# Performance work log

Hardware: AMD Instinct MI355X
Metric: run time of the kernel (lower is better)

## Reference

```python
import jax, jax.numpy as jnp
import numpy as np


def setup_inputs() -> dict:
    key = jax.random.key(0)
    ks = jax.random.split(key, 6)
    b, c, h, w = 8, 256, 48, 48
    return {
        "qry_fts": jax.random.normal(ks[0], (b, c, h, w), dtype=jnp.float32),
        "mask_fts": jax.random.normal(ks[1], (b, c, h, w), dtype=jnp.float32),
        "fts": jax.random.normal(ks[2], (b, c, h, w), dtype=jnp.float32),
        "Wq": jax.random.normal(ks[3], (c, c), dtype=jnp.float32) * (1.0 / np.sqrt(c)),
        "Wk": jax.random.normal(ks[4], (c, c), dtype=jnp.float32) * (1.0 / np.sqrt(c)),
        "Wv": jax.random.normal(ks[5], (c, c), dtype=jnp.float32) * (1.0 / np.sqrt(c)),
        "mu": jnp.full((1,), 0.5, dtype=jnp.float32),
    }


def reference(qry_fts, mask_fts, fts, Wq, Wk, Wv, mu):
    b, c, h, w = qry_fts.shape
    # flatten spatial dims to tokens: [b, N, c], N = h*w
    q_tok = qry_fts.reshape(b, c, h * w).transpose(0, 2, 1)
    m_tok = mask_fts.reshape(b, c, h * w).transpose(0, 2, 1)
    f_tok = fts.reshape(b, c, h * w).transpose(0, 2, 1)

    # torch Linear(no bias): y = x @ W^T with W [out,in]
    Q = jnp.einsum("bnc,dc->bnd", q_tok, Wq)
    K1 = jnp.einsum("bnc,dc->bnd", f_tok, Wk)
    K2 = jnp.einsum("bnc,dc->bnd", m_tok, Wk)
    V = jnp.einsum("bnc,dc->bnd", f_tok, Wv)

    A1 = jax.nn.softmax(jnp.einsum("bqd,bkd->bqk", Q, K1), axis=-1)
    A2 = jax.nn.softmax(jnp.einsum("bqd,bkd->bqk", Q, K2), axis=-1)
    A = (A1 * 0.5 + A2 * mu[0]) / (0.5 + mu[0])

    att = jnp.einsum("bqk,bkd->bqd", A, V)  # [b, N, c]
    att = att.reshape(b, h, w, c).transpose(0, 3, 1, 2)
    return qry_fts + att
```

## Files before the change

kernel.cpp:

```cpp
#include <hip/hip_runtime.h>
#include <math.h>

#define BB 8
#define CC 256
#define NTOK 2304
#define NP 72
#define LOG2E 1.4426950408889634f
#define BIAS2 72.134752f

typedef __attribute__((ext_vector_type(4))) float f32x4;
typedef __attribute__((ext_vector_type(8))) short s16x8;
typedef __attribute__((ext_vector_type(4))) short s16x4;

__device__ inline unsigned short f2bf(float x) {
  unsigned u = __builtin_bit_cast(unsigned, x);
  return (unsigned short)((u + 0x7FFFu + ((u >> 16) & 1u)) >> 16);
}
__device__ inline unsigned short f2h(float x) {
  _Float16 h = (_Float16)x;
  return __builtin_bit_cast(unsigned short, h);
}

__device__ inline void async16(void* lds, const void* g) {
  __builtin_amdgcn_global_load_lds(
      (const __attribute__((address_space(1))) unsigned int*)g,
      (__attribute__((address_space(3))) unsigned int*)lds, 16, 0, 0);
}

__global__ __launch_bounds__(256)
void prep_kernel(const float* __restrict__ X, unsigned short* __restrict__ Xt) {
  __shared__ float Ls[64][65];
  const int t = threadIdx.x;
  const int n0 = blockIdx.x * 64, c0 = blockIdx.y * 64, b = blockIdx.z;
  const float* Xb = X + (size_t)b * CC * NTOK;
  unsigned short* Yb = Xt + (size_t)b * CC * NTOK;

  #pragma unroll
  for (int rr = 0; rr < 16; rr++) {
    int cl = rr * 4 + (t >> 6);
    Ls[cl][t & 63] = Xb[(size_t)(c0 + cl) * NTOK + n0 + (t & 63)];
  }
  __syncthreads();
  #pragma unroll
  for (int rr = 0; rr < 8; rr++) {
    int nl = rr * 8 + (t >> 5);
    int cl = (t & 31) * 2;
    unsigned v = (unsigned)f2h(Ls[cl][nl]) | ((unsigned)f2h(Ls[cl + 1][nl]) << 16);
    *(unsigned*)((char*)Yb + ((size_t)(n0 + nl) * CC + c0 + cl) * 2) = v;
  }
}

__global__ __launch_bounds__(256)
void wconv_kernel(const float* __restrict__ Wq, const float* __restrict__ Wk,
                  const float* __restrict__ Wv, unsigned short* __restrict__ Wqh,
                  unsigned short* __restrict__ Wkh, unsigned short* __restrict__ Wvh) {
  const float* src = (blockIdx.y == 0) ? Wq : (blockIdx.y == 1) ? Wk : Wv;
  unsigned short* dst = (blockIdx.y == 0) ? Wqh : (blockIdx.y == 1) ? Wkh : Wvh;
  int gi = (blockIdx.x * 256 + threadIdx.x) * 4;
  f32x4 v = *(const f32x4*)(src + gi);
  s16x4 o;
  #pragma unroll
  for (int i = 0; i < 4; i++) o[i] = (short)f2h(v[i]);
  *(s16x4*)(dst + gi) = o;
}

template<int MODE>
__global__ __launch_bounds__(256, 2)
void gemm_kernel(const unsigned short* __restrict__ Xt, const unsigned short* __restrict__ Wh,
                 unsigned short* __restrict__ Y) {
  __shared__ alignas(16) char smem[32768];

  const int t = threadIdx.x;
  const int w = t >> 6, l = t & 63, g = l >> 4, c = l & 15;
  const int bid = blockIdx.x;
  const int b = bid & 7, nt = bid >> 3;
  const int n0w = nt * 64 + w * 16;
  const size_t bo = (size_t)b * CC * NTOK;

  const char* Xb = (const char*)(Xt + bo);
  const char* Wb = (const char*)Wh;
  char* Yb = (char*)(Y + (MODE == 2 ? bo : bo));

  int koff[4], cdst[4];
  #pragma unroll
  for (int j = 0; j < 4; j++) {
    int ck = w + 4 * j;
    int row = ck * 2 + (l >> 5);
    koff[j] = row * 512 + (((l & 31) * 16) ^ ((row & 7) << 4));
    cdst[j] = ck * 1024 + l * 16;
  }
  int kxor[8];
  #pragma unroll
  for (int dc = 0; dc < 8; dc++)
    kxor[dc] = (dc * 64 + g * 16) ^ ((c & 7) << 4);

  s16x8 xa[8];
  #pragma unroll
  for (int dc = 0; dc < 8; dc++)
    xa[dc] = *(const s16x8*)(Xb + (n0w + c) * 512 + dc * 64 + g * 16);

  f32x4 acc[16];

#define STAGE_W(WB, TILE)                                            \
  do {                                                               \
    _Pragma("unroll")                                                \
    for (int j_ = 0; j_ < 4; j_++)                                   \
      async16((WB) + cdst[j_], Wb + (TILE) * 16384 + koff[j_]);      \
  } while (0)

  STAGE_W(smem, 0);
  __syncthreads();

  #pragma unroll
  for (int ph = 0; ph < 8; ph++) {
    char* cur = smem + (ph & 1) * 16384;
    if (ph < 7) STAGE_W(smem + ((ph & 1) ^ 1) * 16384, ph + 1);
    __builtin_amdgcn_s_setprio(1);
    #pragma unroll
    for (int s = 0; s < 2; s++) {
      const char* Kt = cur + (s * 16 + c) * 512;
      f32x4 sa = (f32x4){0.f, 0.f, 0.f, 0.f};
      #pragma unroll
      for (int dc = 0; dc < 8; dc++) {
        s16x8 wf = *(const s16x8*)(Kt + kxor[dc]);
        sa = __builtin_amdgcn_mfma_f32_16x16x32_f16(xa[dc], wf, sa, 0, 0, 0);
      }
      acc[ph * 2 + s] = sa;
    }
    __builtin_amdgcn_s_setprio(0);
    __syncthreads();
  }
#undef STAGE_W

  if (MODE == 0 || MODE == 1) {
    unsigned short* Ws = (unsigned short*)(smem + w * 8192);
    #pragma unroll
    for (int dt = 0; dt < 16; dt++)
      #pragma unroll
      for (int j = 0; j < 4; j++) {
        float v = (MODE == 0) ? acc[dt][j] * LOG2E : acc[dt][j];
        Ws[(g * 4 + j) * 256 + dt * 16 + c] = f2h(v);
      }
    #pragma unroll
    for (int r = 0; r < 16; r++) {
      s16x4 v = *(const s16x4*)&Ws[r * 256 + l * 4];
      *(s16x4*)(Yb + (size_t)(n0w + r) * 512 + l * 8) = v;
    }
  } else {
    unsigned short* Vs = (unsigned short*)(smem + w * 8192);
    #pragma unroll
    for (int dt = 0; dt < 16; dt++) {
      s16x4 pv;
      #pragma unroll
      for (int j = 0; j < 4; j++) pv[j] = (short)f2bf(acc[dt][j]);
      *(s16x4*)&Vs[c * 20 + g * 4] = pv;
      s16x4 vv = *(const s16x4*)&Vs[(l >> 2) * 20 + (l & 3) * 4];
      *(s16x4*)(Yb + (size_t)(dt * 16 + (l >> 2)) * 4608 + (size_t)(n0w + (l & 3) * 4) * 2) = vv;
    }
  }
}

__global__ __launch_bounds__(256, 2)
void attn_kernel(const unsigned short* __restrict__ Qf, const unsigned short* __restrict__ K1,
                 const unsigned short* __restrict__ K2, const unsigned short* __restrict__ Vt,
                 const float* __restrict__ qry, const float* __restrict__ mup,
                 float* __restrict__ out) {
  __shared__ alignas(16) char smem[79360];
  char* const kb0 = smem;
  char* const kb1 = smem + 16384;

  const int t = threadIdx.x;
  const int w = t >> 6, l = t & 63, g = l >> 4, c = l & 15;
  const int bid = blockIdx.x;
  const int b = bid & 7, qt = bid >> 3;
  const int q0 = qt * 64 + w * 16;
  const size_t bo = (size_t)b * CC * NTOK;

  const char* Qb  = (const char*)(Qf + bo);
  const char* K1b = (const char*)(K1 + bo);
  const char* K2b = (const char*)(K2 + bo);
  const char* Vtb = (const char*)(Vt + bo);

  float* const Pe0 = (float*)(smem + 65536 + w * 3456);
  float* const Pe1 = Pe0 + 288;
  float* const Pod = Pe0 + 576;

  int koff[2], voff[2], cdst[2];
  #pragma unroll
  for (int j = 0; j < 2; j++) {
    int ck = w + 4 * j;
    int tok = ck * 2 + (l >> 5);
    koff[j] = tok * 512 + (((l & 31) * 16) ^ ((tok & 7) << 4));
    voff[j] = (ck * 32 + (l >> 1)) * 4608 + (l & 1) * 16;
    cdst[j] = ck * 1024 + l * 16;
  }

  int kxor[8];
  #pragma unroll
  for (int dc = 0; dc < 8; dc++)
    kxor[dc] = (dc * 64 + g * 16) ^ ((c & 7) << 4);

  s16x8 qf[8];
  #pragma unroll
  for (int dc = 0; dc < 8; dc++)
    qf[dc] = *(const s16x8*)(Qb + (q0 + c) * 512 + dc * 64 + g * 16);

  f32x4 a1[16], a2[16];
  #pragma unroll
  for (int dt = 0; dt < 16; dt++) {
    a1[dt] = (f32x4){0.f, 0.f, 0.f, 0.f};
    a2[dt] = (f32x4){0.f, 0.f, 0.f, 0.f};
  }
  float lr1[4] = {0.f, 0.f, 0.f, 0.f};
  float lr2[4] = {0.f, 0.f, 0.f, 0.f};

#define STAGE_K(KB, TILE)                                                  \
  do {                                                                     \
    _Pragma("unroll")                                                      \
    for (int pp_ = 0; pp_ < 2; pp_++) {                                    \
      const char* ks_ = (pp_ ? K2b : K1b) + (size_t)(TILE) * 8192;         \
      async16((KB) + pp_ * 8192 + cdst[0], ks_ + koff[0]);                 \
      async16((KB) + pp_ * 8192 + cdst[1], ks_ + koff[1]);                 \
    }                                                                      \
  } while (0)

#define STAGE_V(VB, PAIR)                                                  \
  do {                                                                     \
    _Pragma("unroll")                                                      \
    for (int h_ = 0; h_ < 2; h_++) {                                       \
      const char* vs_ = Vtb + (PAIR) * 64 + h_ * 32;                       \
      async16((VB) + h_ * 8192 + cdst[0], vs_ + voff[0]);                  \
      async16((VB) + h_ * 8192 + cdst[1], vs_ + voff[1]);                  \
    }                                                                      \
  } while (0)

  STAGE_K(kb0, 0);
  STAGE_V(smem + 32768, 0);
  __syncthreads();

  for (int p = 0; p < NP; p++) {
    char* vcur = smem + 32768 + (p & 1) * 16384;
    char* vnxt = smem + 32768 + ((p & 1) ^ 1) * 16384;

    STAGE_K(kb1, 2 * p + 1);
    #pragma unroll
    for (int pp = 0; pp < 2; pp++) {
      const char* Kt = kb0 + pp * 8192 + c * 512;
      f32x4 s = (f32x4){0.f, 0.f, 0.f, 0.f};
      __builtin_amdgcn_s_setprio(1);
      #pragma unroll
      for (int dc = 0; dc < 8; dc++) {
        s16x8 kf = *(const s16x8*)(Kt + kxor[dc]);
        s = __builtin_amdgcn_mfma_f32_16x16x32_f16(qf[dc], kf, s, 0, 0, 0);
      }
      __builtin_amdgcn_s_setprio(0);
      float* lr = pp ? lr2 : lr1;
      float* Pe = pp ? Pe1 : Pe0;
      #pragma unroll
      for (int j = 0; j < 4; j++) {
        float pv = exp2f(s[j] - BIAS2);
        lr[j] += pv;
        Pe[(g * 4 + j) * 18 + c] = pv;
      }
    }
    __syncthreads();

    if (p + 1 < NP) {
      STAGE_K(kb0, 2 * p + 2);
      STAGE_V(vnxt, p + 1);
    }
    s16x8 pa0, pa1;
    #pragma unroll
    for (int pp = 0; pp < 2; pp++) {
      const char* Kt = kb1 + pp * 8192 + c * 512;
      f32x4 s = (f32x4){0.f, 0.f, 0.f, 0.f};
      __builtin_amdgcn_s_setprio(1);
      #pragma unroll
      for (int dc = 0; dc < 8; dc++) {
        s16x8 kf = *(const s16x8*)(Kt + kxor[dc]);
        s = __builtin_amdgcn_mfma_f32_16x16x32_f16(qf[dc], kf, s, 0, 0, 0);
      }
      __builtin_amdgcn_s_setprio(0);
      float* lr = pp ? lr2 : lr1;
      #pragma unroll
      for (int j = 0; j < 4; j++) {
        float pv = exp2f(s[j] - BIAS2);
        lr[j] += pv;
        Pod[(g * 4 + j) * 18 + c] = pv;
      }
      const float* src = ((g < 2) ? (pp ? Pe1 : Pe0) : Pod) + c * 18 + (g & 1) * 8;
      s16x8 v;
      #pragma unroll
      for (int i = 0; i < 8; i++) v[i] = (short)f2bf(src[i]);
      if (pp == 0) pa0 = v; else pa1 = v;
    }
    {
      const char* vbase = vcur + ((g >= 2) ? 8192 : 0) + c * 32 + (g & 1) * 16;
      __builtin_amdgcn_s_setprio(1);
      #pragma unroll
      for (int dt = 0; dt < 16; dt++) {
        s16x8 vf = *(const s16x8*)(vbase + dt * 512);
        a1[dt] = __builtin_amdgcn_mfma_f32_16x16x32_bf16(pa0, vf, a1[dt], 0, 0, 0);
        a2[dt] = __builtin_amdgcn_mfma_f32_16x16x32_bf16(pa1, vf, a2[dt], 0, 0, 0);
      }
      __builtin_amdgcn_s_setprio(0);
    }
    __syncthreads();
  }
#undef STAGE_K
#undef STAGE_V

  #pragma unroll
  for (int j = 0; j < 4; j++) {
    #pragma unroll
    for (int off = 1; off < 16; off <<= 1) {
      lr1[j] += __shfl_xor(lr1[j], off);
      lr2[j] += __shfl_xor(lr2[j], off);
    }
  }
  const float mu = mup[0];
  const float cw1 = 0.5f / (0.5f + mu);
  const float cw2 = mu / (0.5f + mu);
  float r1[4], r2[4];
  #pragma unroll
  for (int j = 0; j < 4; j++) { r1[j] = cw1 / lr1[j]; r2[j] = cw2 / lr2[j]; }

  float* Ws = (float*)(smem + w * 4352);
  const int q = l & 15, ds = l >> 4;
  #pragma unroll
  for (int ch = 0; ch < 4; ch++) {
    #pragma unroll
    for (int dtp = 0; dtp < 4; dtp++) {
      const int dt = ch * 4 + dtp;
      #pragma unroll
      for (int j = 0; j < 4; j++)
        Ws[(g * 4 + j) * 68 + dtp * 16 + c] = a1[dt][j] * r1[j] + a2[dt][j] * r2[j];
    }
    #pragma unroll
    for (int i = 0; i < 16; i++) {
      int d = ch * 64 + i * 4 + ds;
      size_t gi = bo + (size_t)d * NTOK + q0 + q;
      out[gi] = qry[gi] + Ws[q * 68 + i * 4 + ds];
    }
  }
}

extern "C" void kernel_launch(void* const* d_in, const int* in_sizes, int n_in,
                              void* d_out, int out_size, void* d_ws, size_t ws_size,
                              hipStream_t stream) {
  const float* qry  = (const float*)d_in[0];
  const float* mask = (const float*)d_in[1];
  const float* fts  = (const float*)d_in[2];
  const float* Wq   = (const float*)d_in[3];
  const float* Wk   = (const float*)d_in[4];
  const float* Wv   = (const float*)d_in[5];
  const float* mu   = (const float*)d_in[6];
  float* out = (float*)d_out;

  const size_t SZ = (size_t)BB * CC * NTOK;
  unsigned short* Xtq = (unsigned short*)d_ws;
  unsigned short* Xtm = Xtq + SZ;
  unsigned short* Xtf = Xtq + 2 * SZ;
  unsigned short* Qw  = Xtq + 3 * SZ;
  unsigned short* K1w = Xtq + 4 * SZ;
  unsigned short* K2w = Xtq + 5 * SZ;
  unsigned short* Vtw = Xtq + 6 * SZ;
  unsigned short* Wqh = Xtq + 7 * SZ;
  unsigned short* Wkh = Wqh + CC * CC;
  unsigned short* Wvh = Wkh + CC * CC;

  dim3 pg(NTOK / 64, CC / 64, BB);
  prep_kernel<<<pg, 256, 0, stream>>>(qry,  Xtq);
  prep_kernel<<<pg, 256, 0, stream>>>(mask, Xtm);
  prep_kernel<<<pg, 256, 0, stream>>>(fts,  Xtf);
  wconv_kernel<<<dim3(64, 3), 256, 0, stream>>>(Wq, Wk, Wv, Wqh, Wkh, Wvh);

  const int GG = BB * (NTOK / 64);
  gemm_kernel<0><<<GG, 256, 0, stream>>>(Xtq, Wqh, Qw);
  gemm_kernel<1><<<GG, 256, 0, stream>>>(Xtf, Wkh, K1w);
  gemm_kernel<1><<<GG, 256, 0, stream>>>(Xtm, Wkh, K2w);
  gemm_kernel<2><<<GG, 256, 0, stream>>>(Xtf, Wvh, Vtw);

  attn_kernel<<<GG, 256, 0, stream>>>(Qw, K1w, K2w, Vtw, qry, mu, out);
}
```

Baseline: 256.9 us.

## Split attention over key halves and add a combine kernel

The attention kernel now splits the key range into two halves, which doubles the grid from 288 to 576 blocks and gives better occupancy across the CUs. Each block writes unnormalized partial outputs in bf16 plus row sums to workspace, and a new combine kernel sums the halves, normalizes, mixes the two softmaxes and adds the residual. This works because softmax uses a fixed bias instead of a running max. The V LDS layout also gets an XOR swizzle to cut bank conflicts. The cost is extra global traffic for the partials, one more launch, and a second bf16 rounding of the partial outputs.

```diff
diff --git a/kernel.cpp b/kernel.cpp
--- a/kernel.cpp
+++ b/kernel.cpp
@@ -4,7 +4,7 @@
 #define BB 8
 #define CC 256
 #define NTOK 2304
-#define NP 72
+#define NPL 36
 #define LOG2E 1.4426950408889634f
 #define BIAS2 72.134752f
 
@@ -15,6 +15,9 @@
 __device__ inline unsigned short f2bf(float x) {
   unsigned u = __builtin_bit_cast(unsigned, x);
   return (unsigned short)((u + 0x7FFFu + ((u >> 16) & 1u)) >> 16);
+}
+__device__ inline float bf2f(unsigned short h) {
+  return __builtin_bit_cast(float, (unsigned)h << 16);
 }
 __device__ inline unsigned short f2h(float x) {
   _Float16 h = (_Float16)x;
@@ -79,7 +82,7 @@
 
   const char* Xb = (const char*)(Xt + bo);
   const char* Wb = (const char*)Wh;
-  char* Yb = (char*)(Y + (MODE == 2 ? bo : bo));
+  char* Yb = (char*)(Y + bo);
 
   int koff[4], cdst[4];
   #pragma unroll
@@ -163,8 +166,8 @@
 __global__ __launch_bounds__(256, 2)
 void attn_kernel(const unsigned short* __restrict__ Qf, const unsigned short* __restrict__ K1,
                  const unsigned short* __restrict__ K2, const unsigned short* __restrict__ Vt,
-                 const float* __restrict__ qry, const float* __restrict__ mup,
-                 float* __restrict__ out) {
+                 unsigned short* __restrict__ pa1, unsigned short* __restrict__ pa2,
+                 float* __restrict__ lb) {
   __shared__ alignas(16) char smem[79360];
   char* const kb0 = smem;
   char* const kb1 = smem + 16384;
@@ -172,7 +175,9 @@
   const int t = threadIdx.x;
   const int w = t >> 6, l = t & 63, g = l >> 4, c = l & 15;
   const int bid = blockIdx.x;
-  const int b = bid & 7, qt = bid >> 3;
+  const int b = bid & 7;
+  const int r0 = bid >> 3;
+  const int qt = r0 % 36, half = r0 / 36;
   const int q0 = qt * 64 + w * 16;
   const size_t bo = (size_t)b * CC * NTOK;
 
@@ -191,7 +196,7 @@
     int ck = w + 4 * j;
     int tok = ck * 2 + (l >> 5);
     koff[j] = tok * 512 + (((l & 31) * 16) ^ ((tok & 7) << 4));
-    voff[j] = (ck * 32 + (l >> 1)) * 4608 + (l & 1) * 16;
+    voff[j] = (ck * 32 + (l >> 1)) * 4608 + (((l & 1) ^ ((l >> 3) & 1)) << 4);
     cdst[j] = ck * 1024 + l * 16;
   }
 
@@ -234,15 +239,18 @@
     }                                                                      \
   } while (0)
 
-  STAGE_K(kb0, 0);
-  STAGE_V(smem + 32768, 0);
+  const int tb = half * 72;
+  const int pb = half * 36;
+
+  STAGE_K(kb0, tb);
+  STAGE_V(smem + 32768, pb);
   __syncthreads();
 
-  for (int p = 0; p < NP; p++) {
+  for (int p = 0; p < NPL; p++) {
     char* vcur = smem + 32768 + (p & 1) * 16384;
     char* vnxt = smem + 32768 + ((p & 1) ^ 1) * 16384;
 
-    STAGE_K(kb1, 2 * p + 1);
+    STAGE_K(kb1, tb + 2 * p + 1);
     #pragma unroll
     for (int pp = 0; pp < 2; pp++) {
       const char* Kt = kb0 + pp * 8192 + c * 512;
@@ -265,11 +273,11 @@
     }
     __syncthreads();
 
-    if (p + 1 < NP) {
-      STAGE_K(kb0, 2 * p + 2);
-      STAGE_V(vnxt, p + 1);
-    }
-    s16x8 pa0, pa1;
+    if (p + 1 < NPL) {
+      STAGE_K(kb0, tb + 2 * p + 2);
+      STAGE_V(vnxt, pb + p + 1);
+    }
+    s16x8 pa0, pa1r;
     #pragma unroll
     for (int pp = 0; pp < 2; pp++) {
       const char* Kt = kb1 + pp * 8192 + c * 512;
@@ -292,16 +300,17 @@
       s16x8 v;
       #pragma unroll
       for (int i = 0; i < 8; i++) v[i] = (short)f2bf(src[i]);
-      if (pp == 0) pa0 = v; else pa1 = v;
+      if (pp == 0) pa0 = v; else pa1r = v;
     }
     {
-      const char* vbase = vcur + ((g >= 2) ? 8192 : 0) + c * 32 + (g & 1) * 16;
+      const char* vbase = vcur + ((g >= 2) ? 8192 : 0) + c * 32 +
+                          ((((g & 1) ^ ((c >> 2) & 1))) << 4);
       __builtin_amdgcn_s_setprio(1);
       #pragma unroll
       for (int dt = 0; dt < 16; dt++) {
         s16x8 vf = *(const s16x8*)(vbase + dt * 512);
         a1[dt] = __builtin_amdgcn_mfma_f32_16x16x32_bf16(pa0, vf, a1[dt], 0, 0, 0);
-        a2[dt] = __builtin_amdgcn_mfma_f32_16x16x32_bf16(pa1, vf, a2[dt], 0, 0, 0);
+        a2[dt] = __builtin_amdgcn_mfma_f32_16x16x32_bf16(pa1r, vf, a2[dt], 0, 0, 0);
       }
       __builtin_amdgcn_s_setprio(0);
     }
@@ -318,30 +327,75 @@
       lr2[j] += __shfl_xor(lr2[j], off);
     }
   }
-  const float mu = mup[0];
-  const float cw1 = 0.5f / (0.5f + mu);
-  const float cw2 = mu / (0.5f + mu);
-  float r1[4], r2[4];
-  #pragma unroll
-  for (int j = 0; j < 4; j++) { r1[j] = cw1 / lr1[j]; r2[j] = cw2 / lr2[j]; }
-
+  const int pqidx = (half * 8 + b) * 36 + qt;
+  if (c == 0) {
+    #pragma unroll
+    for (int j = 0; j < 4; j++) {
+      int row = w * 16 + g * 4 + j;
+      lb[pqidx * 64 + row] = lr1[j];
+      lb[36864 + pqidx * 64 + row] = lr2[j];
+    }
+  }
+
+  unsigned short* const pb1 = pa1 + (size_t)pqidx * 16384;
+  unsigned short* const pb2 = pa2 + (size_t)pqidx * 16384;
   float* Ws = (float*)(smem + w * 4352);
   const int q = l & 15, ds = l >> 4;
   #pragma unroll
   for (int ch = 0; ch < 4; ch++) {
     #pragma unroll
-    for (int dtp = 0; dtp < 4; dtp++) {
-      const int dt = ch * 4 + dtp;
-      #pragma unroll
-      for (int j = 0; j < 4; j++)
-        Ws[(g * 4 + j) * 68 + dtp * 16 + c] = a1[dt][j] * r1[j] + a2[dt][j] * r2[j];
-    }
-    #pragma unroll
-    for (int i = 0; i < 16; i++) {
-      int d = ch * 64 + i * 4 + ds;
-      size_t gi = bo + (size_t)d * NTOK + q0 + q;
-      out[gi] = qry[gi] + Ws[q * 68 + i * 4 + ds];
-    }
+    for (int pth = 0; pth < 2; pth++) {
+      const f32x4* ap = pth ? a2 : a1;
+      unsigned short* pdst = pth ? pb2 : pb1;
+      #pragma unroll
+      for (int dtp = 0; dtp < 4; dtp++) {
+        const int dt = ch * 4 + dtp;
+        #pragma unroll
+        for (int j = 0; j < 4; j++)
+          Ws[(g * 4 + j) * 68 + dtp * 16 + c] = ap[dt][j];
+      }
+      #pragma unroll
+      for (int i = 0; i < 16; i++) {
+        int d = ch * 64 + i * 4 + ds;
+        pdst[d * 64 + w * 16 + q] = f2bf(Ws[q * 68 + i * 4 + ds]);
+      }
+      __builtin_amdgcn_s_barrier();
+    }
+  }
+}
+
+__global__ __launch_bounds__(256)
+void combine_kernel(const unsigned short* __restrict__ pa1, const unsigned short* __restrict__ pa2,
+                    const float* __restrict__ lb, const float* __restrict__ qry,
+                    const float* __restrict__ mup, float* __restrict__ out) {
+  const int bid = blockIdx.x;
+  const int b = bid & 7, qt = bid >> 3;
+  const int t = threadIdx.x;
+  const int q = t & 63, dr = t >> 6;
+  const size_t bo = (size_t)b * CC * NTOK;
+  const int q0 = qt * 64;
+
+  const int i0 = (0 * 8 + b) * 36 + qt;
+  const int i1 = (1 * 8 + b) * 36 + qt;
+  float l1 = lb[i0 * 64 + q] + lb[i1 * 64 + q];
+  float l2 = lb[36864 + i0 * 64 + q] + lb[36864 + i1 * 64 + q];
+  const float mu = mup[0];
+  const float w1 = 0.5f / (0.5f + mu) / l1;
+  const float w2 = mu / (0.5f + mu) / l2;
+
+  const unsigned short* p10 = pa1 + (size_t)i0 * 16384;
+  const unsigned short* p11 = pa1 + (size_t)i1 * 16384;
+  const unsigned short* p20 = pa2 + (size_t)i0 * 16384;
+  const unsigned short* p21 = pa2 + (size_t)i1 * 16384;
+
+  #pragma unroll
+  for (int i = 0; i < 64; i++) {
+    int d = dr * 64 + i;
+    int off = d * 64 + q;
+    float av1 = bf2f(p10[off]) + bf2f(p11[off]);
+    float av2 = bf2f(p20[off]) + bf2f(p21[off]);
+    size_t gi = bo + (size_t)d * NTOK + q0 + q;
+    out[gi] = qry[gi] + av1 * w1 + av2 * w2;
   }
 }
 
@@ -358,14 +412,18 @@
   float* out = (float*)d_out;
 
   const size_t SZ = (size_t)BB * CC * NTOK;
-  unsigned short* Xtq = (unsigned short*)d_ws;
-  unsigned short* Xtm = Xtq + SZ;
-  unsigned short* Xtf = Xtq + 2 * SZ;
-  unsigned short* Qw  = Xtq + 3 * SZ;
-  unsigned short* K1w = Xtq + 4 * SZ;
-  unsigned short* K2w = Xtq + 5 * SZ;
-  unsigned short* Vtw = Xtq + 6 * SZ;
-  unsigned short* Wqh = Xtq + 7 * SZ;
+  unsigned short* base = (unsigned short*)d_ws;
+  unsigned short* PA1 = base;
+  unsigned short* PA2 = base + 9437184;
+  float*          LB  = (float*)(base + 18874368);
+  unsigned short* Xtq = base;
+  unsigned short* Xtm = base + SZ;
+  unsigned short* Xtf = base + 2 * SZ;
+  unsigned short* Qw  = base + 19169280;
+  unsigned short* K1w = Qw + SZ;
+  unsigned short* K2w = Qw + 2 * SZ;
+  unsigned short* Vtw = Qw + 3 * SZ;
+  unsigned short* Wqh = Qw + 4 * SZ;
   unsigned short* Wkh = Wqh + CC * CC;
   unsigned short* Wvh = Wkh + CC * CC;
 
@@ -381,5 +439,6 @@
   gemm_kernel<1><<<GG, 256, 0, stream>>>(Xtm, Wkh, K2w);
   gemm_kernel<2><<<GG, 256, 0, stream>>>(Xtf, Wvh, Vtw);
 
-  attn_kernel<<<GG, 256, 0, stream>>>(Qw, K1w, K2w, Vtw, qry, mu, out);
-}
+  attn_kernel<<<2 * GG, 256, 0, stream>>>(Qw, K1w, K2w, Vtw, PA1, PA2, LB);
+  combine_kernel<<<GG, 256, 0, stream>>>(PA1, PA2, LB, qry, mu, out);
+}
```

Measured after the change: 258.6 us. No clear change (+0.7%).
